# Kernel tuning notes

Measured on AMD Instinct MI355X. Metric: run time of the kernel, lower is better.

Reference implementation:

```python
import jax, jax.numpy as jnp
import numpy as np

B, T, D = 16, 2048, 1024
NUM_LAYERS = 4
BN_EPS = 1e-5


def setup_inputs() -> dict:
    key = jax.random.key(0)
    ks = jax.random.split(key, 8)
    s = 1.0 / np.sqrt(D)
    x = jax.random.normal(ks[0], (B, T, D), dtype=jnp.float32)
    Wi = jax.random.normal(ks[1], (D, D), dtype=jnp.float32) * s   # SimpleCell input dense kernel
    bi = jnp.zeros((D,), dtype=jnp.float32)                         # SimpleCell input dense bias
    Wh = jax.random.normal(ks[2], (D, D), dtype=jnp.float32) * s   # recurrent dense kernel (no bias)
    mlp_W = jax.random.normal(ks[3], (NUM_LAYERS, D, D), dtype=jnp.float32) * s
    mlp_b = jnp.zeros((NUM_LAYERS, D), dtype=jnp.float32)
    bn_scale = jnp.ones((NUM_LAYERS, D), dtype=jnp.float32)
    bn_bias = jnp.zeros((NUM_LAYERS, D), dtype=jnp.float32)
    return {"x": x, "Wi": Wi, "bi": bi, "Wh": Wh,
            "mlp_W": mlp_W, "mlp_b": mlp_b,
            "bn_scale": bn_scale, "bn_bias": bn_bias}


def reference(x, Wi, bi, Wh, mlp_W, mlp_b, bn_scale, bn_bias):
    # --- linear recurrence (SimpleCell with identity activation) ---
    # h_t = (x_t @ Wi + bi) + h_{t-1} @ Wh,  h_0 = 0
    xp = jnp.einsum('btd,dh->bth', x, Wi) + bi          # pre-project inputs [B,T,H]

    def step(h, xt):
        h = xt + h @ Wh
        return h, h

    h0 = jnp.zeros((x.shape[0], Wh.shape[0]), dtype=x.dtype)
    _, ys = jax.lax.scan(step, h0, jnp.swapaxes(xp, 0, 1))  # scan over time
    y = jnp.swapaxes(ys, 0, 1)                               # [B,T,H]

    # --- residual MLP stack: gelu(BatchNorm(Linear(y))) + y ---
    n_layers = mlp_W.shape[0]
    for l in range(n_layers):
        z = jnp.einsum('bth,hk->btk', y, mlp_W[l]) + mlp_b[l]
        mean = jnp.mean(z, axis=(0, 1))
        var = jnp.var(z, axis=(0, 1))
        zn = (z - mean) * jax.lax.rsqrt(var + BN_EPS) * bn_scale[l] + bn_bias[l]
        y = jax.nn.gelu(zn) + y
    return y
```

## Files before the change

kernel.cpp:

```cpp
#include <hip/hip_runtime.h>
#include <math.h>

#define Bb   16
#define Tt   2048
#define Dd   1024
#define NL   4
#define MTOT (Bb * Tt)

typedef float f32x4 __attribute__((ext_vector_type(4)));
typedef short bf16x8 __attribute__((ext_vector_type(8)));

__device__ __forceinline__ unsigned short f2bf_rne(float x) {
    unsigned u = __float_as_uint(x);
    u += 0x7fffu + ((u >> 16) & 1u);
    return (unsigned short)(u >> 16);
}
__device__ __forceinline__ float bf2f(unsigned short h) {
    return __uint_as_float(((unsigned)h) << 16);
}
__device__ __forceinline__ float gelu_tanh(float x) {
    float x3 = x * x * x;
    float u  = 0.7978845608028654f * (x + 0.044715f * x3);
    return 0.5f * x * (1.0f + tanhf(u));
}
__device__ __forceinline__ void dma16(const void* g, void* l) {
    __builtin_amdgcn_global_load_lds(
        (const __attribute__((address_space(1))) unsigned int*)g,
        (__attribute__((address_space(3))) unsigned int*)l, 16, 0, 0);
}

__global__ __launch_bounds__(256)
void split_bt(const float* __restrict__ B, short* __restrict__ ht,
              short* __restrict__ lt)
{
    __shared__ float tile[32][33];
    const int t  = threadIdx.x;
    const int r  = t >> 3;
    const int c  = (t & 7) * 4;
    const int kb = blockIdx.y * 32;
    const int nb = blockIdx.x * 32;
    float4 v = *reinterpret_cast<const float4*>(
        &B[(size_t)(kb + r) * Dd + nb + c]);
    tile[r][c + 0] = v.x; tile[r][c + 1] = v.y;
    tile[r][c + 2] = v.z; tile[r][c + 3] = v.w;
    __syncthreads();
    unsigned h[4], lo[4];
#pragma unroll
    for (int q = 0; q < 4; ++q) {
        float f = tile[c + q][r];
        unsigned short hh = f2bf_rne(f);
        float rem = f - bf2f(hh);
        h[q]  = hh;
        lo[q] = f2bf_rne(rem);
    }
    uint2 hw, lw;
    hw.x = h[0]  | (h[1]  << 16); hw.y = h[2]  | (h[3]  << 16);
    lw.x = lo[0] | (lo[1] << 16); lw.y = lo[2] | (lo[3] << 16);
    const int n = nb + r;
    const int s = (c >> 3) ^ ((n >> 1) & 3);
    size_t off = ((size_t)(blockIdx.y * 1024 + n) * 4 + s) * 8 + (c & 4);
    *reinterpret_cast<uint2*>(&ht[off]) = hw;
    *reinterpret_cast<uint2*>(&lt[off]) = lw;
}

template<int MODE, int BN, int NT, int S3, int WSPLIT>
__device__ __forceinline__ void gemm_body(
    short* lds, int bx, int by,
    const float* __restrict__ Af,
    const short* __restrict__ Bth, const short* __restrict__ Btl,
    const float* __restrict__ bias,
    const float* __restrict__ Sin,
    float* __restrict__ Cf,
    short* __restrict__ Woh, short* __restrict__ Wol,
    float* __restrict__ psum, float* __restrict__ psq,
    int m, int tstart)
{
    constexpr int NJ    = NT / 32;
    constexpr int APL   = 5120;
    constexpr int BBASE = (S3 ? 2 : 1) * APL;
    constexpr int BPL   = NT * 32;

    const int tid  = threadIdx.x;
    const int lane = tid & 63;
    const int w    = tid >> 6;
    const int n0   = bx * NT;
    const int m0g  = (MODE == 2) ? (by * Tt + tstart) : (by * 128);
    const int wm0  = (w >> 1) * 64;
    const int wn0  = (w & 1) * (NT / 2);
    const int ln   = lane & 15;
    const int ar   = tid >> 3;
    const int ac   = (tid & 7) * 4;

    int  arow_src[4]; bool avalid[4];
#pragma unroll
    for (int p = 0; p < 4; ++p) {
        int rg = m0g + p * 32 + ar;
        bool v = true;
        if (MODE == 1) v = ((rg & (Tt - 1)) >= m);
        avalid[p]   = v;
        arow_src[p] = (MODE >= 1 && v) ? (rg - m) : rg;
    }

    f32x4 acc[4][NJ];
#pragma unroll
    for (int i = 0; i < 4; ++i)
#pragma unroll
        for (int j = 0; j < NJ; ++j) acc[i][j] = (f32x4){0.f, 0.f, 0.f, 0.f};

    int a_off[4];
#pragma unroll
    for (int i = 0; i < 4; ++i)
        a_off[i] = (wm0 + i * 16 + ln) * 40 + (lane >> 4) * 8;
    const int nlb    = wn0 + ln;
    const int b_off0 = BBASE + nlb * 32 +
                       (((lane >> 4) ^ ((nlb >> 1) & 3)) << 3);

    for (int kt = 0; kt < 32; ++kt) {
        __syncthreads();
#pragma unroll
        for (int p = 0; p < 4; ++p) {
            float4 v = *reinterpret_cast<const float4*>(
                &Af[(size_t)arow_src[p] * Dd + kt * 32 + ac]);
            if (MODE == 1 && !avalid[p]) v = make_float4(0.f, 0.f, 0.f, 0.f);
            int wo = (p * 32 + ar) * 40 + ac;
            unsigned short h0 = f2bf_rne(v.x), h1 = f2bf_rne(v.y),
                           h2 = f2bf_rne(v.z), h3 = f2bf_rne(v.w);
            uint2 hw;
            hw.x = (unsigned)h0 | ((unsigned)h1 << 16);
            hw.y = (unsigned)h2 | ((unsigned)h3 << 16);
            *reinterpret_cast<uint2*>(&lds[wo]) = hw;
            if (S3) {
                unsigned short g0 = f2bf_rne(v.x - bf2f(h0)),
                               g1 = f2bf_rne(v.y - bf2f(h1)),
                               g2 = f2bf_rne(v.z - bf2f(h2)),
                               g3 = f2bf_rne(v.w - bf2f(h3));
                uint2 lw;
                lw.x = (unsigned)g0 | ((unsigned)g1 << 16);
                lw.y = (unsigned)g2 | ((unsigned)g3 << 16);
                *reinterpret_cast<uint2*>(&lds[wo + APL]) = lw;
            }
        }
#pragma unroll
        for (int q = 0; q < NT / 64; ++q) {
            size_t gfo = ((size_t)(kt * 1024 + n0 + q * 64 + (tid >> 2))
                          * 4 + (tid & 3)) * 8;
            dma16(&Bth[gfo], &lds[BBASE + q * 2048 + w * 512]);
            if (S3)
                dma16(&Btl[gfo], &lds[BBASE + BPL + q * 2048 + w * 512]);
        }
        __syncthreads();
        bf16x8 ah[4], al[4];
#pragma unroll
        for (int i = 0; i < 4; ++i) {
            ah[i] = *reinterpret_cast<const bf16x8*>(&lds[a_off[i]]);
            if (S3)
                al[i] = *reinterpret_cast<const bf16x8*>(&lds[a_off[i] + APL]);
        }
#pragma unroll
        for (int j = 0; j < NJ; ++j) {
            const bf16x8 bh = *reinterpret_cast<const bf16x8*>(
                &lds[b_off0 + j * 512]);
#pragma unroll
            for (int i = 0; i < 4; ++i)
                acc[i][j] = __builtin_amdgcn_mfma_f32_16x16x32_bf16(
                    ah[i], bh, acc[i][j], 0, 0, 0);
            if (S3) {
                const bf16x8 bl = *reinterpret_cast<const bf16x8*>(
                    &lds[b_off0 + j * 512 + BPL]);
#pragma unroll
                for (int i = 0; i < 4; ++i) {
                    acc[i][j] = __builtin_amdgcn_mfma_f32_16x16x32_bf16(
                        ah[i], bl, acc[i][j], 0, 0, 0);
                    acc[i][j] = __builtin_amdgcn_mfma_f32_16x16x32_bf16(
                        al[i], bh, acc[i][j], 0, 0, 0);
                }
            }
        }
    }

    float* bnF = reinterpret_cast<float*>(lds);
    if (BN) {
        __syncthreads();
        bnF[tid] = 0.f; bnF[256 + tid] = 0.f;
        __syncthreads();
    }
#pragma unroll
    for (int j = 0; j < NJ; ++j) {
        int cl  = wn0 + j * 16 + ln;
        int col = n0 + cl;
        float bj = (MODE == 0 && bias) ? bias[col] : 0.f;
        float sv = 0.f, sq = 0.f;
#pragma unroll
        for (int i = 0; i < 4; ++i) {
            int rbase = m0g + wm0 + i * 16 + (lane >> 4) * 4;
            float vv[4];
#pragma unroll
            for (int e = 0; e < 4; ++e) {
                size_t off = (size_t)(rbase + e) * Dd + col;
                float v = acc[i][j][e] + bj;
                if (MODE >= 1) v += Sin[off];
                Cf[off] = v;
                vv[e] = v;
                if (BN) { sv += v; sq += v * v; }
            }
            if (WSPLIT) {
                unsigned short h0 = f2bf_rne(vv[0]), h1 = f2bf_rne(vv[1]),
                               h2 = f2bf_rne(vv[2]), h3 = f2bf_rne(vv[3]);
                unsigned short l0 = f2bf_rne(vv[0] - bf2f(h0)),
                               l1 = f2bf_rne(vv[1] - bf2f(h1)),
                               l2 = f2bf_rne(vv[2] - bf2f(h2)),
                               l3 = f2bf_rne(vv[3] - bf2f(h3));
                uint2 hw, lw;
                hw.x = (unsigned)h0 | ((unsigned)h1 << 16);
                hw.y = (unsigned)h2 | ((unsigned)h3 << 16);
                lw.x = (unsigned)l0 | ((unsigned)l1 << 16);
                lw.y = (unsigned)l2 | ((unsigned)l3 << 16);
                int kt2 = rbase >> 5;
                int sl  = (rbase >> 3) & 3;
                int e0  = rbase & 7;
                size_t so = ((size_t)(kt2 * 1024 + col) * 4 +
                             (sl ^ ((col >> 1) & 3))) * 8 + e0;
                *reinterpret_cast<uint2*>(&Woh[so]) = hw;
                *reinterpret_cast<uint2*>(&Wol[so]) = lw;
            }
        }
        if (BN) { atomicAdd(&bnF[cl], sv); atomicAdd(&bnF[256 + cl], sq); }
    }
    if (BN) {
        __syncthreads();
        psum[(size_t)by * Dd + n0 + tid] = bnF[tid];
        psq [(size_t)by * Dd + n0 + tid] = bnF[256 + tid];
    }
}

template<int MODE, int BN, int NT, int S3>
__global__ __launch_bounds__(256, 2)
void mfma_gemm(const float* __restrict__ Af,
               const short* __restrict__ Bth, const short* __restrict__ Btl,
               const float* __restrict__ bias,
               const float* __restrict__ Sin,
               float* __restrict__ Cf,
               float* __restrict__ psum, float* __restrict__ psq,
               int m, int tstart)
{
    constexpr int LSZ = (S3 ? 2 : 1) * (5120 + NT * 32);
    __shared__ __align__(16) short lds[LSZ];
    gemm_body<MODE, BN, NT, S3, 0>(lds, blockIdx.x, blockIdx.y,
                                   Af, Bth, Btl, bias, Sin, Cf,
                                   nullptr, nullptr, psum, psq, m, tstart);
}

__global__ __launch_bounds__(256, 2)
void fused_ls(const float* __restrict__ Sfrom, float* __restrict__ Sto,
              const float* __restrict__ Pfrom, float* __restrict__ Pto,
              const short* __restrict__ Bqh, const short* __restrict__ Bql,
              short* __restrict__ Bqoh, short* __restrict__ Bqol,
              int m)
{
    __shared__ __align__(16) short lds[2 * (5120 + 8192)];
    if (blockIdx.y < 16) {
        int sq  = blockIdx.y;
        int sbx = blockIdx.x + ((sq & 1) << 2);
        int sby = sq >> 1;
        gemm_body<0, 0, 128, 1, 1>(lds, sbx, sby, Pfrom, Bqh, Bql,
                                   nullptr, nullptr, Pto, Bqoh, Bqol,
                                   nullptr, nullptr, 0, 0);
    } else {
        gemm_body<1, 0, 256, 1, 0>(lds, blockIdx.x, blockIdx.y - 16,
                                   Sfrom, Bqh, Bql, nullptr, Sfrom, Sto,
                                   nullptr, nullptr, nullptr, nullptr, m, 0);
    }
}

__global__ __launch_bounds__(256)
void bn_stats(const float* __restrict__ ps, const float* __restrict__ pq,
              const float* __restrict__ scale, const float* __restrict__ bias,
              float* __restrict__ Av, float* __restrict__ Cv)
{
    const int d = blockIdx.x * 256 + threadIdx.x;
    float s = 0.f, q = 0.f;
    for (int p = 0; p < 256; ++p) {
        s += ps[p * Dd + d];
        q += pq[p * Dd + d];
    }
    const float invN = 1.0f / 32768.0f;
    float mean = s * invN;
    float var  = q * invN - mean * mean;
    float rs   = rsqrtf(var + 1e-5f);
    float a    = rs * scale[d];
    Av[d] = a;
    Cv[d] = bias[d] - mean * a;
}

__global__ __launch_bounds__(256)
void residual_gelu(const float* __restrict__ Z, const float* __restrict__ Yin,
                   float* __restrict__ Yout,
                   const float* __restrict__ Av, const float* __restrict__ Cv)
{
    const float4* z4 = reinterpret_cast<const float4*>(Z);
    const float4* y4 = reinterpret_cast<const float4*>(Yin);
    float4*       o4 = reinterpret_cast<float4*>(Yout);
    const float4* a4 = reinterpret_cast<const float4*>(Av);
    const float4* c4 = reinterpret_cast<const float4*>(Cv);
    const int n4 = MTOT * Dd / 4;
    for (int i = blockIdx.x * blockDim.x + threadIdx.x; i < n4;
         i += gridDim.x * blockDim.x) {
        int d4 = i & (Dd / 4 - 1);
        float4 z = z4[i], y = y4[i], a = a4[d4], c = c4[d4];
        float4 o;
        o.x = gelu_tanh(fmaf(z.x, a.x, c.x)) + y.x;
        o.y = gelu_tanh(fmaf(z.y, a.y, c.y)) + y.y;
        o.z = gelu_tanh(fmaf(z.z, a.z, c.z)) + y.z;
        o.w = gelu_tanh(fmaf(z.w, a.w, c.w)) + y.w;
        o4[i] = o;
    }
}

extern "C" void kernel_launch(void* const* d_in, const int* in_sizes, int n_in,
                              void* d_out, int out_size, void* d_ws, size_t ws_size,
                              hipStream_t stream)
{
    const float* x    = (const float*)d_in[0];
    const float* Wi   = (const float*)d_in[1];
    const float* bi   = (const float*)d_in[2];
    const float* Wh   = (const float*)d_in[3];
    const float* mlpW = (const float*)d_in[4];
    const float* mlpb = (const float*)d_in[5];
    const float* bns  = (const float*)d_in[6];
    const float* bnb  = (const float*)d_in[7];
    float* out = (float*)d_out;

    const size_t NE = (size_t)MTOT * Dd;
    const size_t MM = (size_t)Dd * Dd;
    float* ws   = (float*)d_ws;
    float* S0   = ws;
    float* Pa   = S0 + NE;
    float* Pb   = Pa + MM;
    float* psum = Pb + MM;
    float* psq  = psum + 256 * Dd;
    float* abuf = psq + 256 * Dd;
    float* cbuf = abuf + Dd;
    short* Bq0h = (short*)(cbuf + Dd);
    short* Bq0l = Bq0h + MM;
    short* Bq1h = Bq0l + MM;
    short* Bq1l = Bq1h + MM;
    short* BmH[NL]; short* BmL[NL];
    {
        short* p = Bq1l + MM;
        for (int l = 0; l < NL; ++l) { BmH[l] = p; p += MM; BmL[l] = p; p += MM; }
    }

    const dim3 gBig(4, 256);
    const dim3 gF  (4, 272);
    const dim3 gSeq(8, 16);
    const dim3 gBt (32, 32);

    split_bt<<<gBt, 256, 0, stream>>>(Wi, Bq0h, Bq0l);
    split_bt<<<gBt, 256, 0, stream>>>(Wh, Bq1h, Bq1l);
    for (int l = 0; l < NL; ++l)
        split_bt<<<gBt, 256, 0, stream>>>(mlpW + (size_t)l * MM, BmH[l], BmL[l]);

    mfma_gemm<0, 0, 256, 1><<<gBig, 256, 0, stream>>>(
        x, Bq0h, Bq0l, bi, nullptr, S0, nullptr, nullptr, 0, 0);

    fused_ls<<<gF, 256, 0, stream>>>(S0, out, Wh, Pa, Bq1h, Bq1l, Bq0h, Bq0l, 1);
    fused_ls<<<gF, 256, 0, stream>>>(out, S0, Pa, Pb, Bq0h, Bq0l, Bq1h, Bq1l, 2);
    fused_ls<<<gF, 256, 0, stream>>>(S0, out, Pb, Pa, Bq1h, Bq1l, Bq0h, Bq0l, 4);
    fused_ls<<<gF, 256, 0, stream>>>(out, S0, Pa, Pb, Bq0h, Bq0l, Bq1h, Bq1l, 8);
    fused_ls<<<gF, 256, 0, stream>>>(S0, out, Pb, Pa, Bq1h, Bq1l, Bq0h, Bq0l, 16);
    fused_ls<<<gF, 256, 0, stream>>>(out, S0, Pa, Pb, Bq0h, Bq0l, Bq1h, Bq1l, 32);
    fused_ls<<<gF, 256, 0, stream>>>(S0, out, Pb, Pa, Bq1h, Bq1l, Bq0h, Bq0l, 64);

    for (int i = 1; i < 16; ++i)
        mfma_gemm<2, 0, 128, 1><<<gSeq, 256, 0, stream>>>(
            out, Bq0h, Bq0l, nullptr, out, out, nullptr, nullptr, 128, 128 * i);

    for (int l = 0; l < NL; ++l) {
        mfma_gemm<0, 1, 256, 0><<<gBig, 256, 0, stream>>>(
            out, BmH[l], BmL[l], mlpb + (size_t)l * Dd, nullptr, S0,
            psum, psq, 0, 0);
        bn_stats<<<4, 256, 0, stream>>>(psum, psq, bns + (size_t)l * Dd,
                                        bnb + (size_t)l * Dd, abuf, cbuf);
        residual_gelu<<<2048, 256, 0, stream>>>(S0, out, out, abuf, cbuf);
    }
}
```

Before: 3.751 ms.

## Replace fifteen carry-propagation launches with one persistent kernel using grid barrier

The sequential carry stage across time chunks was launched as fifteen separate small GEMM kernels. It now runs as one kernel of 128 blocks that loops over the chunks and synchronises between steps through an atomic counter spin barrier, zeroed by a memset. This removes per-launch overhead and the gaps between launches on a small grid. It depends on all 128 blocks being resident at the same time; if they are not, the barrier can deadlock.

```diff
diff --git a/kernel.cpp b/kernel.cpp
--- a/kernel.cpp
+++ b/kernel.cpp
@@ -241,13 +241,13 @@
                const float* __restrict__ Sin,
                float* __restrict__ Cf,
                float* __restrict__ psum, float* __restrict__ psq,
-               int m, int tstart)
+               int m)
 {
     constexpr int LSZ = (S3 ? 2 : 1) * (5120 + NT * 32);
     __shared__ __align__(16) short lds[LSZ];
     gemm_body<MODE, BN, NT, S3, 0>(lds, blockIdx.x, blockIdx.y,
                                    Af, Bth, Btl, bias, Sin, Cf,
-                                   nullptr, nullptr, psum, psq, m, tstart);
+                                   nullptr, nullptr, psum, psq, m, 0);
 }
 
 __global__ __launch_bounds__(256, 2)
@@ -269,6 +269,32 @@
         gemm_body<1, 0, 256, 1, 0>(lds, blockIdx.x, blockIdx.y - 16,
                                    Sfrom, Bqh, Bql, nullptr, Sfrom, Sto,
                                    nullptr, nullptr, nullptr, nullptr, m, 0);
+    }
+}
+
+__global__ __launch_bounds__(256, 2)
+void carry_chain(float* __restrict__ S,
+                 const short* __restrict__ Bth, const short* __restrict__ Btl,
+                 unsigned* __restrict__ cnt)
+{
+    __shared__ __align__(16) short lds[2 * 5120 + 2 * 4096];
+    for (int i = 1; i < 16; ++i) {
+        gemm_body<2, 0, 128, 1, 0>(lds, blockIdx.x, blockIdx.y,
+                                   S, Bth, Btl, nullptr, S, S,
+                                   nullptr, nullptr, nullptr, nullptr,
+                                   128, 128 * i);
+        if (i < 15) {
+            __threadfence();
+            __syncthreads();
+            if (threadIdx.x == 0) {
+                atomicAdd(cnt, 1u);
+                const unsigned tgt = 128u * (unsigned)i;
+                while (atomicOr(cnt, 0u) < tgt)
+                    __builtin_amdgcn_s_sleep(16);
+            }
+            __syncthreads();
+            __threadfence();
+        }
     }
 }
 
@@ -345,10 +371,9 @@
     short* Bq1h = Bq0l + MM;
     short* Bq1l = Bq1h + MM;
     short* BmH[NL]; short* BmL[NL];
-    {
-        short* p = Bq1l + MM;
-        for (int l = 0; l < NL; ++l) { BmH[l] = p; p += MM; BmL[l] = p; p += MM; }
-    }
+    short* p = Bq1l + MM;
+    for (int l = 0; l < NL; ++l) { BmH[l] = p; p += MM; BmL[l] = p; p += MM; }
+    unsigned* bar = (unsigned*)p;
 
     const dim3 gBig(4, 256);
     const dim3 gF  (4, 272);
@@ -359,9 +384,10 @@
     split_bt<<<gBt, 256, 0, stream>>>(Wh, Bq1h, Bq1l);
     for (int l = 0; l < NL; ++l)
         split_bt<<<gBt, 256, 0, stream>>>(mlpW + (size_t)l * MM, BmH[l], BmL[l]);
+    hipMemsetAsync(bar, 0, 8, stream);
 
     mfma_gemm<0, 0, 256, 1><<<gBig, 256, 0, stream>>>(
-        x, Bq0h, Bq0l, bi, nullptr, S0, nullptr, nullptr, 0, 0);
+        x, Bq0h, Bq0l, bi, nullptr, S0, nullptr, nullptr, 0);
 
     fused_ls<<<gF, 256, 0, stream>>>(S0, out, Wh, Pa, Bq1h, Bq1l, Bq0h, Bq0l, 1);
     fused_ls<<<gF, 256, 0, stream>>>(out, S0, Pa, Pb, Bq0h, Bq0l, Bq1h, Bq1l, 2);
@@ -371,14 +397,12 @@
     fused_ls<<<gF, 256, 0, stream>>>(out, S0, Pa, Pb, Bq0h, Bq0l, Bq1h, Bq1l, 32);
     fused_ls<<<gF, 256, 0, stream>>>(S0, out, Pb, Pa, Bq1h, Bq1l, Bq0h, Bq0l, 64);
 
-    for (int i = 1; i < 16; ++i)
-        mfma_gemm<2, 0, 128, 1><<<gSeq, 256, 0, stream>>>(
-            out, Bq0h, Bq0l, nullptr, out, out, nullptr, nullptr, 128, 128 * i);
+    carry_chain<<<gSeq, 256, 0, stream>>>(out, Bq0h, Bq0l, bar);
 
     for (int l = 0; l < NL; ++l) {
         mfma_gemm<0, 1, 256, 0><<<gBig, 256, 0, stream>>>(
             out, BmH[l], BmL[l], mlpb + (size_t)l * Dd, nullptr, S0,
-            psum, psq, 0, 0);
+            psum, psq, 0);
         bn_stats<<<4, 256, 0, stream>>>(psum, psq, bns + (size_t)l * Dd,
                                         bnb + (size_t)l * Dd, abuf, cbuf);
         residual_gelu<<<2048, 256, 0, stream>>>(S0, out, out, abuf, cbuf);
```

After: 4.129 ms. +10.1%, slower.

## Add dedicated 512-thread MLP GEMM kernel with fused BN partial stats

Applied to the files above, without the earlier changes.

Replaces the generic templated GEMM used for the four MLP layers with a specialized kernel that runs 512 threads (8 waves, each owning a 64x64 sub-tile), loads A with wider 8-element vectors, and uses a single bf16 pass with no low-part split. The BN partial-sum reduction moves into this new kernel and the BN template parameter is removed from the shared GEMM body. The aim is more waves per block for latency hiding and simpler per-thread loads in the MLP GEMMs. The cost is more threads contending on the LDS atomics and higher register pressure under the 512-thread launch bound.

```diff
diff --git a/kernel.cpp b/kernel.cpp
--- a/kernel.cpp
+++ b/kernel.cpp
@@ -63,7 +63,7 @@
     *reinterpret_cast<uint2*>(&lt[off]) = lw;
 }
 
-template<int MODE, int BN, int NT, int S3, int WSPLIT>
+template<int MODE, int NT, int S3, int WSPLIT>
 __device__ __forceinline__ void gemm_body(
     short* lds, int bx, int by,
     const float* __restrict__ Af,
@@ -72,7 +72,6 @@
     const float* __restrict__ Sin,
     float* __restrict__ Cf,
     short* __restrict__ Woh, short* __restrict__ Wol,
-    float* __restrict__ psum, float* __restrict__ psq,
     int m, int tstart)
 {
     constexpr int NJ    = NT / 32;
@@ -178,18 +177,11 @@
         }
     }
 
-    float* bnF = reinterpret_cast<float*>(lds);
-    if (BN) {
-        __syncthreads();
-        bnF[tid] = 0.f; bnF[256 + tid] = 0.f;
-        __syncthreads();
-    }
 #pragma unroll
     for (int j = 0; j < NJ; ++j) {
         int cl  = wn0 + j * 16 + ln;
         int col = n0 + cl;
         float bj = (MODE == 0 && bias) ? bias[col] : 0.f;
-        float sv = 0.f, sq = 0.f;
 #pragma unroll
         for (int i = 0; i < 4; ++i) {
             int rbase = m0g + wm0 + i * 16 + (lane >> 4) * 4;
@@ -201,7 +193,6 @@
                 if (MODE >= 1) v += Sin[off];
                 Cf[off] = v;
                 vv[e] = v;
-                if (BN) { sv += v; sq += v * v; }
             }
             if (WSPLIT) {
                 unsigned short h0 = f2bf_rne(vv[0]), h1 = f2bf_rne(vv[1]),
@@ -224,30 +215,23 @@
                 *reinterpret_cast<uint2*>(&Wol[so]) = lw;
             }
         }
-        if (BN) { atomicAdd(&bnF[cl], sv); atomicAdd(&bnF[256 + cl], sq); }
-    }
-    if (BN) {
-        __syncthreads();
-        psum[(size_t)by * Dd + n0 + tid] = bnF[tid];
-        psq [(size_t)by * Dd + n0 + tid] = bnF[256 + tid];
-    }
-}
-
-template<int MODE, int BN, int NT, int S3>
+    }
+}
+
+template<int MODE, int NT, int S3>
 __global__ __launch_bounds__(256, 2)
 void mfma_gemm(const float* __restrict__ Af,
                const short* __restrict__ Bth, const short* __restrict__ Btl,
                const float* __restrict__ bias,
                const float* __restrict__ Sin,
                float* __restrict__ Cf,
-               float* __restrict__ psum, float* __restrict__ psq,
                int m, int tstart)
 {
     constexpr int LSZ = (S3 ? 2 : 1) * (5120 + NT * 32);
     __shared__ __align__(16) short lds[LSZ];
-    gemm_body<MODE, BN, NT, S3, 0>(lds, blockIdx.x, blockIdx.y,
-                                   Af, Bth, Btl, bias, Sin, Cf,
-                                   nullptr, nullptr, psum, psq, m, tstart);
+    gemm_body<MODE, NT, S3, 0>(lds, blockIdx.x, blockIdx.y,
+                               Af, Bth, Btl, bias, Sin, Cf,
+                               nullptr, nullptr, m, tstart);
 }
 
 __global__ __launch_bounds__(256, 2)
@@ -262,13 +246,117 @@
         int sq  = blockIdx.y;
         int sbx = blockIdx.x + ((sq & 1) << 2);
         int sby = sq >> 1;
-        gemm_body<0, 0, 128, 1, 1>(lds, sbx, sby, Pfrom, Bqh, Bql,
-                                   nullptr, nullptr, Pto, Bqoh, Bqol,
-                                   nullptr, nullptr, 0, 0);
+        gemm_body<0, 128, 1, 1>(lds, sbx, sby, Pfrom, Bqh, Bql,
+                                nullptr, nullptr, Pto, Bqoh, Bqol, 0, 0);
     } else {
-        gemm_body<1, 0, 256, 1, 0>(lds, blockIdx.x, blockIdx.y - 16,
-                                   Sfrom, Bqh, Bql, nullptr, Sfrom, Sto,
-                                   nullptr, nullptr, nullptr, nullptr, m, 0);
+        gemm_body<1, 256, 1, 0>(lds, blockIdx.x, blockIdx.y - 16,
+                                Sfrom, Bqh, Bql, nullptr, Sfrom, Sto,
+                                nullptr, nullptr, m, 0);
+    }
+}
+
+__global__ __launch_bounds__(512, 2)
+void mlp_gemm(const float* __restrict__ Af,
+              const short* __restrict__ Bth,
+              const float* __restrict__ bias,
+              float* __restrict__ Cf,
+              float* __restrict__ psum, float* __restrict__ psq)
+{
+    constexpr int APL = 5120;
+    constexpr int BB  = APL;
+    __shared__ __align__(16) short lds[APL + 8192];
+
+    const int tid  = threadIdx.x;
+    const int lane = tid & 63;
+    const int w    = tid >> 6;
+    const int n0   = blockIdx.x * 256;
+    const int m0g  = blockIdx.y * 128;
+    const int wm0  = (w >> 2) * 64;
+    const int wn0  = (w & 3) * 64;
+    const int ln   = lane & 15;
+    const int ar   = tid >> 2;
+    const int ac   = (tid & 3) * 8;
+
+    f32x4 acc[4][4];
+#pragma unroll
+    for (int i = 0; i < 4; ++i)
+#pragma unroll
+        for (int j = 0; j < 4; ++j) acc[i][j] = (f32x4){0.f, 0.f, 0.f, 0.f};
+
+    int a_off[4];
+#pragma unroll
+    for (int i = 0; i < 4; ++i)
+        a_off[i] = (wm0 + i * 16 + ln) * 40 + (lane >> 4) * 8;
+    const int nlb    = wn0 + ln;
+    const int b_off0 = BB + nlb * 32 +
+                       (((lane >> 4) ^ ((nlb >> 1) & 3)) << 3);
+
+    for (int kt = 0; kt < 32; ++kt) {
+        __syncthreads();
+        {
+            const float* p = &Af[(size_t)(m0g + ar) * Dd + kt * 32 + ac];
+            float4 v0 = *reinterpret_cast<const float4*>(p);
+            float4 v1 = *reinterpret_cast<const float4*>(p + 4);
+            unsigned short h0 = f2bf_rne(v0.x), h1 = f2bf_rne(v0.y),
+                           h2 = f2bf_rne(v0.z), h3 = f2bf_rne(v0.w),
+                           h4 = f2bf_rne(v1.x), h5 = f2bf_rne(v1.y),
+                           h6 = f2bf_rne(v1.z), h7 = f2bf_rne(v1.w);
+            int4 hw;
+            hw.x = (int)((unsigned)h0 | ((unsigned)h1 << 16));
+            hw.y = (int)((unsigned)h2 | ((unsigned)h3 << 16));
+            hw.z = (int)((unsigned)h4 | ((unsigned)h5 << 16));
+            hw.w = (int)((unsigned)h6 | ((unsigned)h7 << 16));
+            *reinterpret_cast<int4*>(&lds[ar * 40 + ac]) = hw;
+        }
+#pragma unroll
+        for (int q = 0; q < 2; ++q) {
+            size_t gfo = ((size_t)(kt * 1024 + n0 + q * 128 + (tid >> 2))
+                          * 4 + (tid & 3)) * 8;
+            dma16(&Bth[gfo], &lds[BB + q * 4096 + w * 512]);
+        }
+        __syncthreads();
+        bf16x8 ah[4];
+#pragma unroll
+        for (int i = 0; i < 4; ++i)
+            ah[i] = *reinterpret_cast<const bf16x8*>(&lds[a_off[i]]);
+#pragma unroll
+        for (int j = 0; j < 4; ++j) {
+            const bf16x8 bh = *reinterpret_cast<const bf16x8*>(
+                &lds[b_off0 + j * 512]);
+#pragma unroll
+            for (int i = 0; i < 4; ++i)
+                acc[i][j] = __builtin_amdgcn_mfma_f32_16x16x32_bf16(
+                    ah[i], bh, acc[i][j], 0, 0, 0);
+        }
+    }
+
+    float* bnF = reinterpret_cast<float*>(lds);
+    __syncthreads();
+    if (tid < 256) { bnF[tid] = 0.f; bnF[256 + tid] = 0.f; }
+    __syncthreads();
+#pragma unroll
+    for (int j = 0; j < 4; ++j) {
+        int cl  = wn0 + j * 16 + ln;
+        int col = n0 + cl;
+        float bj = bias[col];
+        float sv = 0.f, sq = 0.f;
+#pragma unroll
+        for (int i = 0; i < 4; ++i) {
+            int rbase = m0g + wm0 + i * 16 + (lane >> 4) * 4;
+#pragma unroll
+            for (int e = 0; e < 4; ++e) {
+                size_t off = (size_t)(rbase + e) * Dd + col;
+                float v = acc[i][j][e] + bj;
+                Cf[off] = v;
+                sv += v; sq += v * v;
+            }
+        }
+        atomicAdd(&bnF[cl], sv); atomicAdd(&bnF[256 + cl], sq);
+    }
+    __syncthreads();
+    if (tid < 256) {
+        psum[(size_t)blockIdx.y * Dd + n0 + tid] = bnF[tid];
+        psq [(size_t)blockIdx.y * Dd + n0 + tid] = bnF[256 + tid];
     }
 }
 
@@ -360,8 +448,8 @@
     for (int l = 0; l < NL; ++l)
         split_bt<<<gBt, 256, 0, stream>>>(mlpW + (size_t)l * MM, BmH[l], BmL[l]);
 
-    mfma_gemm<0, 0, 256, 1><<<gBig, 256, 0, stream>>>(
-        x, Bq0h, Bq0l, bi, nullptr, S0, nullptr, nullptr, 0, 0);
+    mfma_gemm<0, 256, 1><<<gBig, 256, 0, stream>>>(
+        x, Bq0h, Bq0l, bi, nullptr, S0, 0, 0);
 
     fused_ls<<<gF, 256, 0, stream>>>(S0, out, Wh, Pa, Bq1h, Bq1l, Bq0h, Bq0l, 1);
     fused_ls<<<gF, 256, 0, stream>>>(out, S0, Pa, Pb, Bq0h, Bq0l, Bq1h, Bq1l, 2);
@@ -372,13 +460,12 @@
     fused_ls<<<gF, 256, 0, stream>>>(S0, out, Pb, Pa, Bq1h, Bq1l, Bq0h, Bq0l, 64);
 
     for (int i = 1; i < 16; ++i)
-        mfma_gemm<2, 0, 128, 1><<<gSeq, 256, 0, stream>>>(
-            out, Bq0h, Bq0l, nullptr, out, out, nullptr, nullptr, 128, 128 * i);
+        mfma_gemm<2, 128, 1><<<gSeq, 256, 0, stream>>>(
+            out, Bq0h, Bq0l, nullptr, out, out, 128, 128 * i);
 
     for (int l = 0; l < NL; ++l) {
-        mfma_gemm<0, 1, 256, 0><<<gBig, 256, 0, stream>>>(
-            out, BmH[l], BmL[l], mlpb + (size_t)l * Dd, nullptr, S0,
-            psum, psq, 0, 0);
+        mlp_gemm<<<gBig, 512, 0, stream>>>(
+            out, BmH[l], mlpb + (size_t)l * Dd, S0, psum, psq);
         bn_stats<<<4, 256, 0, stream>>>(psum, psq, bns + (size_t)l * Dd,
                                         bnb + (size_t)l * Dd, abuf, cbuf);
         residual_gelu<<<2048, 256, 0, stream>>>(S0, out, out, abuf, cbuf);
```

After: 3.750 ms. Within noise of the previous version (-0.0%).
